# Optimization experiments

Hardware: AMD Instinct MI355X
Metric: run time of the kernel (lower is better)

Reference implementation:

```python
import jax, jax.numpy as jnp
import numpy as np

INDEX_SHIFT = jnp.array([[0, 0], [-1, 0], [1, 0], [0, 1], [-1, 1], [1, 1], [0, -1], [-1, -1], [1, -1]], dtype=jnp.int32)
GRID = jnp.array([513, 513], dtype=jnp.int32)  # pseudo_image_dims + 1


def setup_inputs() -> dict:
    key = jax.random.key(0)
    k1, k2, k3, k4 = jax.random.split(key, 4)
    li_bev_coors = jax.random.randint(k1, (8192, 2), 0, 512, dtype=jnp.int32)
    ra_bev_coors = jax.random.randint(k2, (2048, 2), 0, 512, dtype=jnp.int32)
    ra_pts = jax.random.normal(k3, (2048, 5), dtype=jnp.float32)
    ra_voxel_coords = jax.random.randint(k4, (2048, 3), 0, 512, dtype=jnp.int32)
    return {"li_bev_coors": li_bev_coors, "ra_bev_coors": ra_bev_coors,
            "ra_pts": ra_pts, "ra_voxel_coords": ra_voxel_coords}


def _neighbour_coors(bev_grids):
    # [N,2] -> [N,9,2]: shift by 9-neighborhood, wrap by (grid_size+1)
    return (bev_grids[:, None, :] + INDEX_SHIFT[None, :, :]) % GRID


def _nearest_dy(neighbour_coor, dy_coor, dy_mask):
    # neighbour_coor: [N,9,2] int; dy_coor: [M,2] float; dy_mask: [M] bool
    n = neighbour_coor.shape[0]
    a = neighbour_coor.reshape(-1, 2).astype(jnp.float32)        # [N*9, 2]
    a2 = jnp.sum(a * a, axis=-1)                                  # [N*9]
    b2 = jnp.sum(dy_coor * dy_coor, axis=-1)                      # [M]
    # squared euclidean distances (exact: integer coordinates)
    d2 = a2[:, None] + b2[None, :] - 2.0 * (a @ dy_coor.T)        # [N*9, M]
    d2 = jnp.where(dy_mask[None, :], d2, jnp.inf)                 # mask non-dynamic voxels
    dmin = jnp.sqrt(jnp.maximum(jnp.min(d2, axis=-1), 0.0))       # min commutes with sqrt
    return (dmin * 0.01).reshape(n, 9)


def reference(li_bev_coors, ra_bev_coors, ra_pts, ra_voxel_coords):
    # dynamic-point selection: |velocity| > 0.1 (column 4)
    dy_mask = jnp.abs(ra_pts[:, 4]) > 0.1                         # [M]
    dy_coor = ra_voxel_coords[:, 1:].astype(jnp.float32)          # [M,2]
    # (uniquifying dy_coor does not change the min-distance; skip for jit shapes)
    li_nb = _neighbour_coors(li_bev_coors)                        # [N_li,9,2]
    ra_nb = _neighbour_coors(ra_bev_coors)                        # [N_ra,9,2]
    use = jnp.sum(dy_mask) > 1
    li_dis = jnp.where(use, _nearest_dy(li_nb, dy_coor, dy_mask), 0.0)
    ra_dis = jnp.where(use, _nearest_dy(ra_nb, dy_coor, dy_mask), 0.0)
    return (li_dis, ra_dis)
```

## Files before the change

kernel.cpp:

```cpp
#include <hip/hip_runtime.h>

#define BLOCK 256
#define SPLITS 32
#define QPT 8
#define MAXC 264


__global__ __launch_bounds__(BLOCK) void partial_kernel(
    const int* __restrict__ li_coors, int n_li,
    const int* __restrict__ ra_coors, int n_ra,
    const float* __restrict__ pts,
    const int* __restrict__ vox,
    int m, int cs, int csPad,
    float* __restrict__ partials,
    int* __restrict__ counts)
{
    __shared__ __align__(16) float2 sc[MAXC];
    __shared__ int s_cnt;

    if (threadIdx.x == 0) s_cnt = 0;
    __syncthreads();

    const int split = blockIdx.y;
    const int base = split * cs;
    int nvalid = 0;
    for (int i = threadIdx.x; i < csPad; i += BLOCK) {
        int gi = base + i;
        float x = 3.0e4f, y = 3.0e4f;
        if (i < cs && gi < m) {
            if (fabsf(pts[gi * 5 + 4]) > 0.1f) {
                x = (float)vox[gi * 3 + 1];
                y = (float)vox[gi * 3 + 2];
                nvalid++;
            }
        }
        sc[i] = make_float2(x, y);
    }
    if (nvalid) atomicAdd(&s_cnt, nvalid);
    __syncthreads();
    if (blockIdx.x == 0 && threadIdx.x == 0) counts[split] = s_cnt;

    const int li_total = n_li * 9;
    const int total = (n_li + n_ra) * 9;
    const int qbase = blockIdx.x * (BLOCK * QPT) + threadIdx.x;

    float n2x[QPT], n2y[QPT], q2[QPT], mn[QPT];
#pragma unroll
    for (int k = 0; k < QPT; ++k) {
        int q = qbase + k * BLOCK;
        float qx = 0.0f, qy = 0.0f;
        if (q < total) {
            const int shift_x[9] = {0,-1,1,0,-1,1,0,-1,1};
            const int shift_y[9] = {0, 0,0,1, 1,1,-1,-1,-1};
            int n, s;
            const int* src;
            if (q < li_total) { n = q / 9; s = q - n * 9; src = li_coors; }
            else { int r = q - li_total; n = r / 9; s = r - n * 9; src = ra_coors; }
            int cx = src[n * 2 + 0] + shift_x[s];
            int cy = src[n * 2 + 1] + shift_y[s];
            if (cx < 0) cx += 513;
            if (cy < 0) cy += 513;
            qx = (float)cx; qy = (float)cy;
        }
        n2x[k] = -2.0f * qx;
        n2y[k] = -2.0f * qy;
        q2[k]  = fmaf(qx, qx, qy * qy);
        mn[k]  = 3.4e38f;
    }

    const float4* __restrict__ s4 = (const float4*)sc;
    const int iters = csPad >> 1;
    for (int i = 0; i < iters; ++i) {
        float4 a = s4[i];
        float c2a = fmaf(a.x, a.x, a.y * a.y);
        float c2b = fmaf(a.z, a.z, a.w * a.w);
#pragma unroll
        for (int k = 0; k < QPT; ++k) {
            float ta = fmaf(a.x, n2x[k], fmaf(a.y, n2y[k], c2a));
            float tb = fmaf(a.z, n2x[k], fmaf(a.w, n2y[k], c2b));
            mn[k] = fminf(fminf(ta, tb), mn[k]);
        }
    }

    float* __restrict__ dst = partials + (size_t)split * total;
#pragma unroll
    for (int k = 0; k < QPT; ++k) {
        int q = qbase + k * BLOCK;
        if (q < total) dst[q] = q2[k] + mn[k];
    }
}

__global__ __launch_bounds__(BLOCK) void finalize_kernel(
    const float* __restrict__ partials, int total,
    const int* __restrict__ counts, float* __restrict__ out)
{
    int q = blockIdx.x * BLOCK + threadIdx.x;
    if (q >= total) return;
    int cnt = 0;
#pragma unroll
    for (int s = 0; s < SPLITS; ++s) cnt += counts[s];
    float best = 3.4e38f;
#pragma unroll
    for (int s = 0; s < SPLITS; ++s)
        best = fminf(best, partials[(size_t)s * total + q]);
    out[q] = (cnt > 1) ? sqrtf(best) * 0.01f : 0.0f;
}

extern "C" void kernel_launch(void* const* d_in, const int* in_sizes, int n_in,
                              void* d_out, int out_size, void* d_ws, size_t ws_size,
                              hipStream_t stream) {
    const int*   li  = (const int*)d_in[0];
    const int*   ra  = (const int*)d_in[1];
    const float* pts = (const float*)d_in[2];
    const int*   vox = (const int*)d_in[3];
    float* out = (float*)d_out;

    const int n_li = in_sizes[0] / 2;
    const int n_ra = in_sizes[1] / 2;
    const int m    = in_sizes[2] / 5;

    const int total = (n_li + n_ra) * 9;
    const int qblocks = (total + BLOCK * QPT - 1) / (BLOCK * QPT);
    const int fblocks = (total + BLOCK - 1) / BLOCK;

    const int cs    = (m + SPLITS - 1) / SPLITS;
    const int csPad = (cs + 7) & ~7;

    float* partials = (float*)d_ws;
    int*   counts   = (int*)((char*)d_ws + (size_t)SPLITS * total * sizeof(float));

    dim3 grid(qblocks, SPLITS);
    partial_kernel<<<grid, BLOCK, 0, stream>>>(li, n_li, ra, n_ra, pts, vox,
                                               m, cs, csPad, partials, counts);
    finalize_kernel<<<fblocks, BLOCK, 0, stream>>>(partials, total, counts, out);
}
```

Measured before the change: 83.21 us.

## Precompute candidate arrays once and reduce splits with atomicMin into output

```diff
diff --git a/kernel.cpp b/kernel.cpp
--- a/kernel.cpp
+++ b/kernel.cpp
@@ -1,47 +1,53 @@
 #include <hip/hip_runtime.h>
 
 #define BLOCK 256
-#define SPLITS 32
+#define SPLITS 16
 #define QPT 8
-#define MAXC 264
+#define PREPT 1024
 
 
-__global__ __launch_bounds__(BLOCK) void partial_kernel(
-    const int* __restrict__ li_coors, int n_li,
-    const int* __restrict__ ra_coors, int n_ra,
-    const float* __restrict__ pts,
-    const int* __restrict__ vox,
-    int m, int cs, int csPad,
-    float* __restrict__ partials,
-    int* __restrict__ counts)
+
+__global__ __launch_bounds__(PREPT) void prep_kernel(
+    const float* __restrict__ pts, const int* __restrict__ vox,
+    int m, int mPad,
+    int* __restrict__ gate, float* __restrict__ wx, float* __restrict__ wy,
+    int* __restrict__ out_bits, int total)
 {
-    __shared__ __align__(16) float2 sc[MAXC];
     __shared__ int s_cnt;
-
     if (threadIdx.x == 0) s_cnt = 0;
     __syncthreads();
 
+    int nv = 0;
+    for (int i = threadIdx.x; i < mPad; i += PREPT) {
+        float x = 3.0e4f, y = 3.0e4f;
+        if (i < m && fabsf(pts[i * 5 + 4]) > 0.1f) {
+            x = (float)vox[i * 3 + 1];
+            y = (float)vox[i * 3 + 2];
+            nv++;
+        }
+        wx[i] = x;
+        wy[i] = y;
+    }
+    if (nv) atomicAdd(&s_cnt, nv);
+
+    const int4 iv = make_int4(0x7F7F7F7F, 0x7F7F7F7F, 0x7F7F7F7F, 0x7F7F7F7F);
+    int4* o4 = (int4*)out_bits;
+    const int n4 = total >> 2;
+    for (int i = threadIdx.x; i < n4; i += PREPT) o4[i] = iv;
+
+    __syncthreads();
+    if (threadIdx.x == 0) *gate = (s_cnt > 1) ? 1 : 0;
+}
+
+__global__ __launch_bounds__(BLOCK) void main_kernel(
+    const int* __restrict__ li_coors, int n_li,
+    const int* __restrict__ ra_coors, int n_ra,
+    const float* __restrict__ wx, const float* __restrict__ wy,
+    const int* __restrict__ gate, int cs,
+    int* __restrict__ out_bits, int total)
+{
     const int split = blockIdx.y;
-    const int base = split * cs;
-    int nvalid = 0;
-    for (int i = threadIdx.x; i < csPad; i += BLOCK) {
-        int gi = base + i;
-        float x = 3.0e4f, y = 3.0e4f;
-        if (i < cs && gi < m) {
-            if (fabsf(pts[gi * 5 + 4]) > 0.1f) {
-                x = (float)vox[gi * 3 + 1];
-                y = (float)vox[gi * 3 + 2];
-                nvalid++;
-            }
-        }
-        sc[i] = make_float2(x, y);
-    }
-    if (nvalid) atomicAdd(&s_cnt, nvalid);
-    __syncthreads();
-    if (blockIdx.x == 0 && threadIdx.x == 0) counts[split] = s_cnt;
-
     const int li_total = n_li * 9;
-    const int total = (n_li + n_ra) * 9;
     const int qbase = blockIdx.x * (BLOCK * QPT) + threadIdx.x;
 
     float n2x[QPT], n2y[QPT], q2[QPT], mn[QPT];
@@ -68,42 +74,37 @@
         mn[k]  = 3.4e38f;
     }
 
-    const float4* __restrict__ s4 = (const float4*)sc;
-    const int iters = csPad >> 1;
+    const float4* __restrict__ X4 = (const float4*)(wx + split * cs);
+    const float4* __restrict__ Y4 = (const float4*)(wy + split * cs);
+    const int iters = cs >> 2;
     for (int i = 0; i < iters; ++i) {
-        float4 a = s4[i];
-        float c2a = fmaf(a.x, a.x, a.y * a.y);
-        float c2b = fmaf(a.z, a.z, a.w * a.w);
+        float4 X = X4[i];
+        float4 Y = Y4[i];
+        float c0 = fmaf(X.x, X.x, Y.x * Y.x);
+        float c1 = fmaf(X.y, X.y, Y.y * Y.y);
+        float c2 = fmaf(X.z, X.z, Y.z * Y.z);
+        float c3 = fmaf(X.w, X.w, Y.w * Y.w);
 #pragma unroll
         for (int k = 0; k < QPT; ++k) {
-            float ta = fmaf(a.x, n2x[k], fmaf(a.y, n2y[k], c2a));
-            float tb = fmaf(a.z, n2x[k], fmaf(a.w, n2y[k], c2b));
-            mn[k] = fminf(fminf(ta, tb), mn[k]);
+            float t0 = fmaf(X.x, n2x[k], fmaf(Y.x, n2y[k], c0));
+            float t1 = fmaf(X.y, n2x[k], fmaf(Y.y, n2y[k], c1));
+            float t2 = fmaf(X.z, n2x[k], fmaf(Y.z, n2y[k], c2));
+            float t3 = fmaf(X.w, n2x[k], fmaf(Y.w, n2y[k], c3));
+            mn[k] = fminf(fminf(t0, t1), mn[k]);
+            mn[k] = fminf(fminf(t2, t3), mn[k]);
         }
     }
 
-    float* __restrict__ dst = partials + (size_t)split * total;
+    const int g = *gate;
 #pragma unroll
     for (int k = 0; k < QPT; ++k) {
         int q = qbase + k * BLOCK;
-        if (q < total) dst[q] = q2[k] + mn[k];
+        if (q < total) {
+            float d2 = q2[k] + mn[k];
+            float val = g ? sqrtf(d2) * 0.01f : 0.0f;
+            atomicMin(out_bits + q, __float_as_int(val));
+        }
     }
-}
-
-__global__ __launch_bounds__(BLOCK) void finalize_kernel(
-    const float* __restrict__ partials, int total,
-    const int* __restrict__ counts, float* __restrict__ out)
-{
-    int q = blockIdx.x * BLOCK + threadIdx.x;
-    if (q >= total) return;
-    int cnt = 0;
-#pragma unroll
-    for (int s = 0; s < SPLITS; ++s) cnt += counts[s];
-    float best = 3.4e38f;
-#pragma unroll
-    for (int s = 0; s < SPLITS; ++s)
-        best = fminf(best, partials[(size_t)s * total + q]);
-    out[q] = (cnt > 1) ? sqrtf(best) * 0.01f : 0.0f;
 }
 
 extern "C" void kernel_launch(void* const* d_in, const int* in_sizes, int n_in,
@@ -113,7 +114,6 @@
     const int*   ra  = (const int*)d_in[1];
     const float* pts = (const float*)d_in[2];
     const int*   vox = (const int*)d_in[3];
-    float* out = (float*)d_out;
 
     const int n_li = in_sizes[0] / 2;
     const int n_ra = in_sizes[1] / 2;
@@ -121,16 +121,18 @@
 
     const int total = (n_li + n_ra) * 9;
     const int qblocks = (total + BLOCK * QPT - 1) / (BLOCK * QPT);
-    const int fblocks = (total + BLOCK - 1) / BLOCK;
 
-    const int cs    = (m + SPLITS - 1) / SPLITS;
-    const int csPad = (cs + 7) & ~7;
+    const int unit = SPLITS * 4;
+    const int mPad = ((m + unit - 1) / unit) * unit;
+    const int cs   = mPad / SPLITS;
 
-    float* partials = (float*)d_ws;
-    int*   counts   = (int*)((char*)d_ws + (size_t)SPLITS * total * sizeof(float));
+    int*   gate = (int*)d_ws;
+    float* wx   = (float*)((char*)d_ws + 256);
+    float* wy   = (float*)((char*)d_ws + 256 + (size_t)mPad * sizeof(float));
+    int*   outb = (int*)d_out;
 
-    dim3 grid(qblocks, SPLITS);
-    partial_kernel<<<grid, BLOCK, 0, stream>>>(li, n_li, ra, n_ra, pts, vox,
-                                               m, cs, csPad, partials, counts);
-    finalize_kernel<<<fblocks, BLOCK, 0, stream>>>(partials, total, counts, out);
+    prep_kernel<<<1, PREPT, 0, stream>>>(pts, vox, m, mPad, gate, wx, wy,
+                                         outb, total);
+    main_kernel<<<dim3(qblocks, SPLITS), BLOCK, 0, stream>>>(
+        li, n_li, ra, n_ra, wx, wy, gate, cs, outb, total);
 }
```

After: 86.00 us. 1.03x slower.
